# Performance work log

Hardware: AMD Instinct MI355X
Metric: run time of the kernel (lower is better)

The kernel has to match this reference:

```python
import jax, jax.numpy as jnp
import numpy as np

N_NODES, D_H, D_MSG, N_LAYERS = 512, 64, 64, 3
T, E = 128, 8192


def setup_inputs() -> dict:
    key = jax.random.key(0)
    ks = jax.random.split(key, 16)
    s = 0.1
    t = jax.random.uniform(ks[0], (T,), dtype=jnp.float32)
    edge_index = jax.random.randint(ks[1], (2, E), 0, N_NODES, dtype=jnp.int64)
    inp = {
        "t": t,
        "edge_index": edge_index,
        "enc_w": jax.random.normal(ks[2], (1 + N_NODES, D_H), jnp.float32) * s,
        "enc_b": jnp.zeros((D_H,), jnp.float32),
        "msg1_w": jax.random.normal(ks[3], (N_LAYERS, 2 * D_H, D_MSG), jnp.float32) * s,
        "msg1_b": jnp.zeros((N_LAYERS, D_MSG), jnp.float32),
        "msg2_w": jax.random.normal(ks[4], (N_LAYERS, D_MSG, D_MSG), jnp.float32) * s,
        "msg2_b": jnp.zeros((N_LAYERS, D_MSG), jnp.float32),
        "upd1_w": jax.random.normal(ks[5], (N_LAYERS, D_H + D_MSG, D_H), jnp.float32) * s,
        "upd1_b": jnp.zeros((N_LAYERS, D_H), jnp.float32),
        "upd2_w": jax.random.normal(ks[6], (N_LAYERS, D_H, D_H), jnp.float32) * s,
        "upd2_b": jnp.zeros((N_LAYERS, D_H), jnp.float32),
        "ro_w": jax.random.normal(ks[7], (D_H, 1), jnp.float32) * s,
        "ro_b": jnp.zeros((1,), jnp.float32),
    }
    return inp


def reference(t, edge_index, enc_w, enc_b, msg1_w, msg1_b, msg2_w, msg2_b,
              upd1_w, upd1_b, upd2_w, upd2_b, ro_w, ro_b):
    Tn = t.shape[0]
    N = enc_w.shape[0] - 1
    L = msg1_w.shape[0]
    # node features: [t, one_hot(node_id)] -> encode
    t_feat = jnp.broadcast_to(t[:, None, None], (Tn, N, 1))          # [T,N,1]
    id_feat = jnp.broadcast_to(jnp.eye(N, dtype=t.dtype), (Tn, N, N))  # [T,N,N]
    x = jnp.concatenate([t_feat, id_feat], axis=-1)                   # [T,N,1+N]
    h = x @ enc_w + enc_b                                             # [T,N,d_h]
    src, dst = edge_index[0], edge_index[1]
    for l in range(L):
        # message MLP on gathered [h_src, h_dst]
        cat = jnp.concatenate([h[:, src], h[:, dst]], axis=-1)        # [T,E,2*d_h]
        m = jax.nn.silu(cat @ msg1_w[l] + msg1_b[l]) @ msg2_w[l] + msg2_b[l]  # [T,E,d_msg]
        # scatter-add into destination nodes (index_add)
        agg = jnp.zeros((Tn, N, m.shape[-1]), dtype=h.dtype).at[:, dst].add(m)
        u = jnp.concatenate([h, agg], axis=-1)                        # [T,N,d_h+d_msg]
        upd = jax.nn.silu(u @ upd1_w[l] + upd1_b[l]) @ upd2_w[l] + upd2_b[l]
        h = h + upd                                                   # residual
    out = (h @ ro_w + ro_b)[..., 0]                                   # [T,N]
    return out
```

## Files before the change

kernel.cpp:

```cpp
#include <hip/hip_runtime.h>

#define TT 128
#define NN 512
#define DH 64
#define EE 8192
#define LOB (18 * 8 * 64)

typedef __bf16 bf16x8 __attribute__((ext_vector_type(8)));
typedef float f32x4 __attribute__((ext_vector_type(4)));

struct US8 { unsigned short u[8]; };
struct Frag { bf16x8 hi, lo; };

static __device__ __forceinline__ unsigned short f2bf(float x) {
    union { float f; unsigned u; } c; c.f = x;
    unsigned r = (c.u + 0x7FFFu + ((c.u >> 16) & 1u)) >> 16;
    return (unsigned short)r;
}
static __device__ __forceinline__ float bf2f(unsigned short b) {
    union { unsigned u; float f; } c; c.u = ((unsigned)b) << 16;
    return c.f;
}
static __device__ __forceinline__ float silu_acc(float a, float b, float acc) {
    float x = a + b;
    float e = __expf(-x);
    return fmaf(x, __builtin_amdgcn_rcpf(1.0f + e), acc);
}
static __device__ __forceinline__ float silu_f(float x) {
    float e = __expf(-x);
    return x * __builtin_amdgcn_rcpf(1.0f + e);
}
static __device__ __forceinline__ Frag split8(const float* v) {
    Frag f;
    #pragma unroll
    for (int i = 0; i < 8; ++i) {
        __bf16 hb = (__bf16)v[i];
        f.hi[i] = hb;
        f.lo[i] = (__bf16)(v[i] - (float)hb);
    }
    return f;
}
static __device__ __forceinline__ f32x4 mmac(bf16x8 a, uint4 bw, f32x4 c) {
    return __builtin_amdgcn_mfma_f32_16x16x32_bf16(
        a, __builtin_bit_cast(bf16x8, bw), c, 0, 0, 0);
}
static __device__ __forceinline__ f32x4 mm3(Frag a, uint4 wh, uint4 wl, f32x4 c) {
    c = mmac(a.hi, wh, c);
    c = mmac(a.lo, wh, c);
    c = mmac(a.hi, wl, c);
    return c;
}

__global__ __launch_bounds__(512) void setup_kernel(
    const int* __restrict__ ei,
    const float* __restrict__ msg1_w, const float* __restrict__ msg2_w,
    const float* __restrict__ upd1_w, const float* __restrict__ upd2_w,
    const float* __restrict__ msg2_b,
    const float* __restrict__ enc_w, const float* __restrict__ enc_b,
    const float* __restrict__ msg1_b,
    uint4* __restrict__ pack,
    int* __restrict__ counts, int* __restrict__ offsets,
    int* __restrict__ ssrc,
    float* __restrict__ E1s, float* __restrict__ E1d,
    float* __restrict__ e0sum, float* __restrict__ c2) {
    int b = blockIdx.x;
    if (b < 18) {
        int l = b / 6, bi = b % 6;
        const float* W;
        if (bi == 0)      W = msg1_w + (size_t)l * 128 * 64;
        else if (bi == 1) W = msg1_w + (size_t)l * 128 * 64 + 64 * 64;
        else if (bi == 3) W = upd1_w + (size_t)l * 128 * 64;
        else if (bi == 4) W = upd1_w + (size_t)l * 128 * 64 + 64 * 64;
        else if (bi == 5) W = upd2_w + (size_t)l * 64 * 64;
        else              W = nullptr;
        __shared__ float Gs[64 * 64];
        if (bi == 2) {
            const float* W2  = msg2_w + (size_t)l * 64 * 64;
            const float* U1b = upd1_w + (size_t)l * 128 * 64 + 64 * 64;
            int k = threadIdx.x >> 3;
            int dbase = (threadIdx.x & 7) * 8;
            float acc[8] = {0.f, 0.f, 0.f, 0.f, 0.f, 0.f, 0.f, 0.f};
            for (int j = 0; j < 64; ++j) {
                float a = W2[k * 64 + j];
                #pragma unroll
                for (int i = 0; i < 8; ++i)
                    acc[i] = fmaf(a, U1b[j * 64 + dbase + i], acc[i]);
            }
            #pragma unroll
            for (int i = 0; i < 8; ++i) Gs[k * 64 + dbase + i] = acc[i];
            if (threadIdx.x < 64) {
                int d = threadIdx.x;
                float s = 0.f;
                for (int j = 0; j < 64; ++j)
                    s = fmaf(msg2_b[l * 64 + j], U1b[j * 64 + d], s);
                c2[l * 64 + d] = s;
            }
            __syncthreads();
            W = Gs;
        }
        int lane = threadIdx.x & 63;
        int sub  = threadIdx.x >> 6;
        int nt = sub >> 1, kc = sub & 1;
        US8 oh, ol;
        #pragma unroll
        for (int i = 0; i < 8; ++i) {
            int k = kc * 32 + (lane >> 4) * 8 + i;
            int col = nt * 16 + (lane & 15);
            float w = W[k * 64 + col];
            unsigned short hu = f2bf(w);
            oh.u[i] = hu;
            ol.u[i] = f2bf(w - bf2f(hu));
        }
        size_t fi = ((size_t)b * 8 + sub) * 64 + lane;
        pack[fi]       = __builtin_bit_cast(uint4, oh);
        pack[LOB + fi] = __builtin_bit_cast(uint4, ol);
        return;
    }
    if (b == 18) {
        __shared__ int cnt[NN];
        __shared__ int tmp[NN];
        __shared__ int cur[NN];
        int i = threadIdx.x;
        cnt[i] = 0;
        __syncthreads();
        #pragma unroll
        for (int r = 0; r < EE / 512; ++r)
            atomicAdd(&cnt[ei[EE + r * 512 + i]], 1);
        __syncthreads();
        int c = cnt[i];
        tmp[i] = c;
        __syncthreads();
        for (int off = 1; off < NN; off <<= 1) {
            int v = (i >= off) ? tmp[i - off] : 0;
            __syncthreads();
            tmp[i] += v;
            __syncthreads();
        }
        counts[i] = c;
        offsets[i + 1] = tmp[i];
        if (i == 0) offsets[0] = 0;
        cur[i] = tmp[i] - c;
        __syncthreads();
        #pragma unroll
        for (int r = 0; r < EE / 512; ++r) {
            int e = r * 512 + i;
            int dst = ei[EE + e];
            int pos = atomicAdd(&cur[dst], 1);
            ssrc[pos] = ei[e];
        }
        return;
    }
    if (b < 83) {
        int nn = (b - 19) * 8 + (threadIdx.x >> 6);
        int d  = threadIdx.x & 63;
        float s = 0.f, dd = msg1_b[d];
        #pragma unroll 8
        for (int k = 0; k < 64; ++k) {
            float c = enc_w[(1 + nn) * 64 + k] + enc_b[k];
            s  = fmaf(c, msg1_w[k * 64 + d], s);
            dd = fmaf(c, msg1_w[(64 + k) * 64 + d], dd);
        }
        E1s[nn * 64 + d] = s;
        E1d[nn * 64 + d] = dd;
        return;
    }
    if (threadIdx.x < 64) {
        int d = threadIdx.x;
        float s = 0.f, dd = 0.f;
        #pragma unroll 8
        for (int k = 0; k < 64; ++k) {
            float a = enc_w[k];
            s  = fmaf(a, msg1_w[k * 64 + d], s);
            dd = fmaf(a, msg1_w[(64 + k) * 64 + d], dd);
        }
        e0sum[d] = s + dd;
    }
}

static __device__ __forceinline__ int swz_rowbase(int bid, int w) {
    int xcd = bid & 7;
    int idx = bid >> 3;
    int tt  = xcd * 16 + (idx >> 3);
    int sub = idx & 7;
    return tt * NN + sub * 64 + w * 16;
}

#define AGG_BODY(GB, BASE)                                                     \
    float4 acc = make_float4(0.f, 0.f, 0.f, 0.f);                              \
    int i = beg + eg;                                                          \
    for (; i + 4 < end; i += 8) {                                              \
        int s0 = ssrc[i] << 8;                                                 \
        int s1 = ssrc[i + 4] << 8;                                             \
        float4 v0 = *(const float4*)(GB + s0 + ch4);                           \
        float4 v1 = *(const float4*)(GB + s1 + ch4);                           \
        acc.x = silu_acc(v0.x, BASE.x, acc.x);                                 \
        acc.y = silu_acc(v0.y, BASE.y, acc.y);                                 \
        acc.z = silu_acc(v0.z, BASE.z, acc.z);                                 \
        acc.w = silu_acc(v0.w, BASE.w, acc.w);                                 \
        acc.x = silu_acc(v1.x, BASE.x, acc.x);                                 \
        acc.y = silu_acc(v1.y, BASE.y, acc.y);                                 \
        acc.z = silu_acc(v1.z, BASE.z, acc.z);                                 \
        acc.w = silu_acc(v1.w, BASE.w, acc.w);                                 \
    }                                                                          \
    if (i < end) {                                                             \
        int s0 = ssrc[i] << 8;                                                 \
        float4 v0 = *(const float4*)(GB + s0 + ch4);                           \
        acc.x = silu_acc(v0.x, BASE.x, acc.x);                                 \
        acc.y = silu_acc(v0.y, BASE.y, acc.y);                                 \
        acc.z = silu_acc(v0.z, BASE.z, acc.z);                                 \
        acc.w = silu_acc(v0.w, BASE.w, acc.w);                                 \
    }                                                                          \
    acc.x += __shfl_xor(acc.x, 16); acc.x += __shfl_xor(acc.x, 32);            \
    acc.y += __shfl_xor(acc.y, 16); acc.y += __shfl_xor(acc.y, 32);            \
    acc.z += __shfl_xor(acc.z, 16); acc.z += __shfl_xor(acc.z, 32);            \
    acc.w += __shfl_xor(acc.w, 16); acc.w += __shfl_xor(acc.w, 32);

__global__ __launch_bounds__(256) void agg0_kernel(
    const float* __restrict__ t, const float* __restrict__ e0sum,
    const float* __restrict__ E1s, const float* __restrict__ E1d,
    const int* __restrict__ offsets, const int* __restrict__ ssrc,
    float* __restrict__ aggpre) {
    int bid = blockIdx.x;
    int xcd = bid & 7;
    int idx = bid >> 3;
    int tt  = xcd * 16 + (idx >> 7);
    int n   = (idx & 127) * 4 + (threadIdx.x >> 6);
    int lane = threadIdx.x & 63;
    int eg = lane >> 4;
    int chb = (lane & 15) * 4;
    int ch4 = chb * 4;
    float tv = t[tt];
    float4 e0 = *(const float4*)(e0sum + chb);
    float4 ed = *(const float4*)(E1d + n * DH + chb);
    float4 base = make_float4(fmaf(tv, e0.x, ed.x), fmaf(tv, e0.y, ed.y),
                              fmaf(tv, e0.z, ed.z), fmaf(tv, e0.w, ed.w));
    int beg = offsets[n], end = offsets[n + 1];
    const char* Eb = (const char*)E1s;
    AGG_BODY(Eb, base)
    if (eg == 0)
        *(float4*)(aggpre + ((size_t)tt * NN + n) * DH + chb) = acc;
}

__global__ __launch_bounds__(256) void agg_kernel(
    const float* __restrict__ hs, const float* __restrict__ hd,
    const int* __restrict__ offsets, const int* __restrict__ ssrc,
    float* __restrict__ aggpre) {
    int bid = blockIdx.x;
    int xcd = bid & 7;
    int idx = bid >> 3;
    int tt  = xcd * 16 + (idx >> 7);
    int n   = (idx & 127) * 4 + (threadIdx.x >> 6);
    int lane = threadIdx.x & 63;
    size_t rowoff = ((size_t)tt * NN + n) * DH;
    int eg = lane >> 4;
    int chb = (lane & 15) * 4;
    int ch4 = chb * 4;
    float4 hdv = *(const float4*)(hd + rowoff + chb);
    int beg = offsets[n], end = offsets[n + 1];
    const char* hb = (const char*)(hs + (size_t)tt * NN * DH);
    AGG_BODY(hb, hdv)
    if (eg == 0) *(float4*)(aggpre + rowoff + chb) = acc;
}

__global__ __launch_bounds__(256) void upd_mfma_kernel(
    float* __restrict__ h, const float* __restrict__ aggpre,
    const float* __restrict__ t, const float* __restrict__ enc_w,
    const float* __restrict__ enc_b,
    const int* __restrict__ counts, const uint4* __restrict__ pack, int l,
    const float* __restrict__ c2, const float* __restrict__ ub1,
    const float* __restrict__ ub2, const float* __restrict__ b1n,
    float* __restrict__ hs, float* __restrict__ hd,
    const float* __restrict__ ro_w, const float* __restrict__ ro_b,
    float* __restrict__ out, int first, int last) {
    __shared__ float tile[4][16 * 68];
    int lane = threadIdx.x & 63;
    int w = threadIdx.x >> 6;
    int rowbase = swz_rowbase(blockIdx.x, w);
    float* TA = tile[w];
    int arow = lane & 15, kgrp = lane >> 4, k0 = kgrp * 8;
    int hrow = rowbase + arow;

    float hf[16];
    if (first) {
        int n = (rowbase & (NN - 1)) + arow;
        float tv = t[rowbase >> 9];
        #pragma unroll
        for (int kc = 0; kc < 2; ++kc)
            #pragma unroll
            for (int i = 0; i < 8; ++i) {
                int k = kc * 32 + k0 + i;
                hf[kc * 8 + i] = tv * enc_w[k] + enc_w[(1 + n) * DH + k] + enc_b[k];
            }
    } else {
        *(float4*)&hf[0]  = *(const float4*)(h + (size_t)hrow * DH + k0);
        *(float4*)&hf[4]  = *(const float4*)(h + (size_t)hrow * DH + k0 + 4);
        *(float4*)&hf[8]  = *(const float4*)(h + (size_t)hrow * DH + 32 + k0);
        *(float4*)&hf[12] = *(const float4*)(h + (size_t)hrow * DH + 32 + k0 + 4);
    }
    Frag ha0 = split8(&hf[0]), ha1 = split8(&hf[8]);

    float gf[16];
    *(float4*)&gf[0]  = *(const float4*)(aggpre + (size_t)hrow * DH + k0);
    *(float4*)&gf[4]  = *(const float4*)(aggpre + (size_t)hrow * DH + k0 + 4);
    *(float4*)&gf[8]  = *(const float4*)(aggpre + (size_t)hrow * DH + 32 + k0);
    *(float4*)&gf[12] = *(const float4*)(aggpre + (size_t)hrow * DH + 32 + k0 + 4);
    Frag ga0 = split8(&gf[0]), ga1 = split8(&gf[8]);

    const uint4* PGH  = pack + (size_t)(l * 6 + 2) * 512;
    const uint4* PGL  = PGH + LOB;
    const uint4* PU1tH = pack + (size_t)(l * 6 + 3) * 512;
    const uint4* PU1tL = PU1tH + LOB;
    const float* c2l = c2 + l * 64;
    float degv[4];
    #pragma unroll
    for (int r = 0; r < 4; ++r)
        degv[r] = (float)counts[(rowbase + kgrp * 4 + r) & (NN - 1)];
    #pragma unroll
    for (int nt = 0; nt < 4; ++nt) {
        float bv  = ub1[nt * 16 + (lane & 15)];
        float c2v = c2l[nt * 16 + (lane & 15)];
        f32x4 a;
        #pragma unroll
        for (int r = 0; r < 4; ++r) a[r] = fmaf(degv[r], c2v, bv);
        a = mm3(ha0, PU1tH[(nt * 2 + 0) * 64 + lane], PU1tL[(nt * 2 + 0) * 64 + lane], a);
        a = mm3(ha1, PU1tH[(nt * 2 + 1) * 64 + lane], PU1tL[(nt * 2 + 1) * 64 + lane], a);
        a = mm3(ga0, PGH[(nt * 2 + 0) * 64 + lane], PGL[(nt * 2 + 0) * 64 + lane], a);
        a = mm3(ga1, PGH[(nt * 2 + 1) * 64 + lane], PGL[(nt * 2 + 1) * 64 + lane], a);
        #pragma unroll
        for (int r = 0; r < 4; ++r)
            TA[(kgrp * 4 + r) * 68 + nt * 16 + (lane & 15)] = silu_f(a[r]);
    }
    float zb[16];
    #pragma unroll
    for (int i = 0; i < 8; ++i) zb[i] = TA[arow * 68 + k0 + i];
    #pragma unroll
    for (int i = 0; i < 8; ++i) zb[8 + i] = TA[arow * 68 + 32 + k0 + i];
    Frag kz0 = split8(&zb[0]), kz1 = split8(&zb[8]);

    const uint4* PU2H = pack + (size_t)(l * 6 + 5) * 512;
    const uint4* PU2L = PU2H + LOB;
    #pragma unroll
    for (int nt = 0; nt < 4; ++nt) {
        float bv = ub2[nt * 16 + (lane & 15)];
        f32x4 a;
        #pragma unroll
        for (int r = 0; r < 4; ++r) a[r] = bv;
        a = mm3(kz0, PU2H[(nt * 2 + 0) * 64 + lane], PU2L[(nt * 2 + 0) * 64 + lane], a);
        a = mm3(kz1, PU2H[(nt * 2 + 1) * 64 + lane], PU2L[(nt * 2 + 1) * 64 + lane], a);
        #pragma unroll
        for (int r = 0; r < 4; ++r)
            TA[(kgrp * 4 + r) * 68 + nt * 16 + (lane & 15)] = a[r];
    }
    float hn[16];
    #pragma unroll
    for (int i = 0; i < 8; ++i) hn[i] = hf[i] + TA[arow * 68 + k0 + i];
    #pragma unroll
    for (int i = 0; i < 8; ++i) hn[8 + i] = hf[8 + i] + TA[arow * 68 + 32 + k0 + i];

    if (last) {
        float v = 0.f;
        #pragma unroll
        for (int i = 0; i < 8; ++i) v += hn[i] * ro_w[k0 + i];
        #pragma unroll
        for (int i = 0; i < 8; ++i) v += hn[8 + i] * ro_w[32 + k0 + i];
        v += __shfl_xor(v, 16);
        v += __shfl_xor(v, 32);
        if (lane < 16) out[rowbase + lane] = v + ro_b[0];
        return;
    }

    *(float4*)(h + (size_t)hrow * DH + k0) = make_float4(hn[0], hn[1], hn[2], hn[3]);
    *(float4*)(h + (size_t)hrow * DH + k0 + 4) = make_float4(hn[4], hn[5], hn[6], hn[7]);
    *(float4*)(h + (size_t)hrow * DH + 32 + k0) = make_float4(hn[8], hn[9], hn[10], hn[11]);
    *(float4*)(h + (size_t)hrow * DH + 32 + k0 + 4) = make_float4(hn[12], hn[13], hn[14], hn[15]);

    Frag na0 = split8(&hn[0]), na1 = split8(&hn[8]);
    const uint4* PWtH = pack + (size_t)((l + 1) * 6 + 0) * 512;
    const uint4* PWbH = pack + (size_t)((l + 1) * 6 + 1) * 512;
    const uint4* PWtL = PWtH + LOB;
    const uint4* PWbL = PWbH + LOB;
    #pragma unroll
    for (int nt = 0; nt < 4; ++nt) {
        f32x4 s; f32x4 d;
        float b1v = b1n[nt * 16 + (lane & 15)];
        #pragma unroll
        for (int r = 0; r < 4; ++r) { s[r] = 0.f; d[r] = b1v; }
        s = mm3(na0, PWtH[(nt * 2 + 0) * 64 + lane], PWtL[(nt * 2 + 0) * 64 + lane], s);
        s = mm3(na1, PWtH[(nt * 2 + 1) * 64 + lane], PWtL[(nt * 2 + 1) * 64 + lane], s);
        d = mm3(na0, PWbH[(nt * 2 + 0) * 64 + lane], PWbL[(nt * 2 + 0) * 64 + lane], d);
        d = mm3(na1, PWbH[(nt * 2 + 1) * 64 + lane], PWbL[(nt * 2 + 1) * 64 + lane], d);
        #pragma unroll
        for (int r = 0; r < 4; ++r) {
            int rr = rowbase + kgrp * 4 + r;
            hs[(size_t)rr * DH + nt * 16 + (lane & 15)] = s[r];
            hd[(size_t)rr * DH + nt * 16 + (lane & 15)] = d[r];
        }
    }
}

extern "C" void kernel_launch(void* const* d_in, const int* in_sizes, int n_in,
                              void* d_out, int out_size, void* d_ws, size_t ws_size,
                              hipStream_t stream) {
    const float* t      = (const float*)d_in[0];
    const int*   ei     = (const int*)d_in[1];
    const float* enc_w  = (const float*)d_in[2];
    const float* enc_b  = (const float*)d_in[3];
    const float* msg1_w = (const float*)d_in[4];
    const float* msg1_b = (const float*)d_in[5];
    const float* msg2_w = (const float*)d_in[6];
    const float* msg2_b = (const float*)d_in[7];
    const float* upd1_w = (const float*)d_in[8];
    const float* upd1_b = (const float*)d_in[9];
    const float* upd2_w = (const float*)d_in[10];
    const float* upd2_b = (const float*)d_in[11];
    const float* ro_w   = (const float*)d_in[12];
    const float* ro_b   = (const float*)d_in[13];
    float* out = (float*)d_out;

    const size_t HN = (size_t)TT * NN * DH;
    float* h      = (float*)d_ws;
    float* hs     = h + HN;
    float* hd     = hs + HN;
    float* aggpre = hd + HN;
    uint4* pack   = (uint4*)(aggpre + HN);
    int* counts  = (int*)(pack + 2 * LOB);
    int* offsets = counts + NN;
    int* ssrc    = offsets + NN + 1;
    float* E1s   = (float*)(ssrc + EE);
    float* E1d   = E1s + NN * DH;
    float* e0sum = E1d + NN * DH;
    float* c2    = e0sum + DH;

    setup_kernel<<<84, 512, 0, stream>>>(ei, msg1_w, msg2_w, upd1_w, upd2_w,
                                         msg2_b, enc_w, enc_b, msg1_b,
                                         pack, counts, offsets, ssrc,
                                         E1s, E1d, e0sum, c2);

    for (int l = 0; l < 3; ++l) {
        if (l == 0)
            agg0_kernel<<<TT * NN / 4, 256, 0, stream>>>(
                t, e0sum, E1s, E1d, offsets, ssrc, aggpre);
        else
            agg_kernel<<<TT * NN / 4, 256, 0, stream>>>(
                hs, hd, offsets, ssrc, aggpre);
        int last = (l == 2);
        upd_mfma_kernel<<<TT * NN / 64, 256, 0, stream>>>(
            h, aggpre, t, enc_w, enc_b, counts, pack, l,
            c2, upd1_b + (size_t)l * DH,
            upd2_b + (size_t)l * DH,
            last ? msg1_b : msg1_b + (size_t)(l + 1) * DH,
            hs, hd, ro_w, ro_b, out, (l == 0) ? 1 : 0, last);
    }
}
```

Measured before the change: 266.6 us.

## Fuse all GNN layers into one persistent cooperative kernel with grid sync

```diff
diff --git a/kernel.cpp b/kernel.cpp
--- a/kernel.cpp
+++ b/kernel.cpp
@@ -1,4 +1,7 @@
 #include <hip/hip_runtime.h>
+#include <hip/hip_cooperative_groups.h>
+
+namespace cg = cooperative_groups;
 
 #define TT 128
 #define NN 512
@@ -215,6 +218,175 @@
     acc.z += __shfl_xor(acc.z, 16); acc.z += __shfl_xor(acc.z, 32);            \
     acc.w += __shfl_xor(acc.w, 16); acc.w += __shfl_xor(acc.w, 32);
 
+__global__ __launch_bounds__(512, 4) void gnn_coop(
+    const float* __restrict__ t, const float* __restrict__ enc_w,
+    const float* __restrict__ enc_b, const uint4* __restrict__ pack,
+    const int* __restrict__ counts, const int* __restrict__ offsets,
+    const int* __restrict__ ssrc,
+    const float* __restrict__ E1s, const float* __restrict__ E1d,
+    const float* __restrict__ e0sum,
+    float* __restrict__ hsA, float* __restrict__ hsB,
+    float* __restrict__ hd,
+    const float* __restrict__ msg1_b, const float* __restrict__ upd1_b,
+    const float* __restrict__ upd2_b, const float* __restrict__ c2,
+    const float* __restrict__ ro_w, const float* __restrict__ ro_b,
+    float* __restrict__ out) {
+    cg::grid_group grid = cg::this_grid();
+    __shared__ float tile[8][16 * 68];
+    int lane = threadIdx.x & 63;
+    int w = threadIdx.x >> 6;
+    int bid = blockIdx.x;
+    int xcd = bid & 7;
+    int idx = bid >> 3;
+    int tt  = xcd * 16 + (idx >> 2);
+    int quarter = idx & 3;
+    int rowbase = tt * NN + quarter * 128 + w * 16;
+    int nbase = rowbase & (NN - 1);
+    float* TA = tile[w];
+    int arow = lane & 15, kgrp = lane >> 4, k0 = kgrp * 8;
+    float tv = t[tt];
+
+    float hv[16];
+    {
+        int n = nbase + arow;
+        #pragma unroll
+        for (int kc = 0; kc < 2; ++kc)
+            #pragma unroll
+            for (int i = 0; i < 8; ++i) {
+                int k = kc * 32 + k0 + i;
+                hv[kc * 8 + i] = tv * enc_w[k] + enc_w[(1 + n) * DH + k] + enc_b[k];
+            }
+    }
+
+    const float* hs_in = hsA;
+    float* hs_out = hsA;
+
+    for (int l = 0; l < 3; ++l) {
+        int first = (l == 0), last = (l == 2);
+
+        {
+            int eg = lane >> 4;
+            int chb = (lane & 15) * 4;
+            int ch4 = chb * 4;
+            const char* gb = first ? (const char*)E1s
+                                   : (const char*)(hs_in + (size_t)tt * NN * DH);
+            for (int j = 0; j < 16; ++j) {
+                int nn = nbase + j;
+                float4 base;
+                if (first) {
+                    float4 e0 = *(const float4*)(e0sum + chb);
+                    float4 ed = *(const float4*)(E1d + nn * DH + chb);
+                    base = make_float4(fmaf(tv, e0.x, ed.x), fmaf(tv, e0.y, ed.y),
+                                       fmaf(tv, e0.z, ed.z), fmaf(tv, e0.w, ed.w));
+                } else {
+                    base = *(const float4*)(hd + ((size_t)tt * NN + nn) * DH + chb);
+                }
+                int beg = offsets[nn], end = offsets[nn + 1];
+                AGG_BODY(gb, base)
+                if (eg == 0) *(float4*)(&TA[j * 68 + chb]) = acc;
+            }
+        }
+
+        float gf[16];
+        #pragma unroll
+        for (int i = 0; i < 8; ++i) gf[i] = TA[arow * 68 + k0 + i];
+        #pragma unroll
+        for (int i = 0; i < 8; ++i) gf[8 + i] = TA[arow * 68 + 32 + k0 + i];
+        Frag ga0 = split8(&gf[0]), ga1 = split8(&gf[8]);
+        Frag ha0 = split8(&hv[0]), ha1 = split8(&hv[8]);
+
+        const uint4* PGH   = pack + (size_t)(l * 6 + 2) * 512;
+        const uint4* PGL   = PGH + LOB;
+        const uint4* PU1tH = pack + (size_t)(l * 6 + 3) * 512;
+        const uint4* PU1tL = PU1tH + LOB;
+        const float* c2l = c2 + l * 64;
+        const float* ub1 = upd1_b + l * 64;
+        float degv[4];
+        #pragma unroll
+        for (int r = 0; r < 4; ++r)
+            degv[r] = (float)counts[nbase + kgrp * 4 + r];
+        #pragma unroll
+        for (int nt = 0; nt < 4; ++nt) {
+            float bv  = ub1[nt * 16 + (lane & 15)];
+            float c2v = c2l[nt * 16 + (lane & 15)];
+            f32x4 a;
+            #pragma unroll
+            for (int r = 0; r < 4; ++r) a[r] = fmaf(degv[r], c2v, bv);
+            a = mm3(ha0, PU1tH[(nt * 2 + 0) * 64 + lane], PU1tL[(nt * 2 + 0) * 64 + lane], a);
+            a = mm3(ha1, PU1tH[(nt * 2 + 1) * 64 + lane], PU1tL[(nt * 2 + 1) * 64 + lane], a);
+            a = mm3(ga0, PGH[(nt * 2 + 0) * 64 + lane], PGL[(nt * 2 + 0) * 64 + lane], a);
+            a = mm3(ga1, PGH[(nt * 2 + 1) * 64 + lane], PGL[(nt * 2 + 1) * 64 + lane], a);
+            #pragma unroll
+            for (int r = 0; r < 4; ++r)
+                TA[(kgrp * 4 + r) * 68 + nt * 16 + (lane & 15)] = silu_f(a[r]);
+        }
+        float zb[16];
+        #pragma unroll
+        for (int i = 0; i < 8; ++i) zb[i] = TA[arow * 68 + k0 + i];
+        #pragma unroll
+        for (int i = 0; i < 8; ++i) zb[8 + i] = TA[arow * 68 + 32 + k0 + i];
+        Frag kz0 = split8(&zb[0]), kz1 = split8(&zb[8]);
+
+        const uint4* PU2H = pack + (size_t)(l * 6 + 5) * 512;
+        const uint4* PU2L = PU2H + LOB;
+        const float* ub2 = upd2_b + l * 64;
+        #pragma unroll
+        for (int nt = 0; nt < 4; ++nt) {
+            float bv = ub2[nt * 16 + (lane & 15)];
+            f32x4 a;
+            #pragma unroll
+            for (int r = 0; r < 4; ++r) a[r] = bv;
+            a = mm3(kz0, PU2H[(nt * 2 + 0) * 64 + lane], PU2L[(nt * 2 + 0) * 64 + lane], a);
+            a = mm3(kz1, PU2H[(nt * 2 + 1) * 64 + lane], PU2L[(nt * 2 + 1) * 64 + lane], a);
+            #pragma unroll
+            for (int r = 0; r < 4; ++r)
+                TA[(kgrp * 4 + r) * 68 + nt * 16 + (lane & 15)] = a[r];
+        }
+        #pragma unroll
+        for (int i = 0; i < 8; ++i) hv[i] += TA[arow * 68 + k0 + i];
+        #pragma unroll
+        for (int i = 0; i < 8; ++i) hv[8 + i] += TA[arow * 68 + 32 + k0 + i];
+
+        if (last) {
+            float v = 0.f;
+            #pragma unroll
+            for (int i = 0; i < 8; ++i) v += hv[i] * ro_w[k0 + i];
+            #pragma unroll
+            for (int i = 0; i < 8; ++i) v += hv[8 + i] * ro_w[32 + k0 + i];
+            v += __shfl_xor(v, 16);
+            v += __shfl_xor(v, 32);
+            if (lane < 16) out[rowbase + lane] = v + ro_b[0];
+        } else {
+            Frag na0 = split8(&hv[0]), na1 = split8(&hv[8]);
+            const uint4* PWtH = pack + (size_t)((l + 1) * 6 + 0) * 512;
+            const uint4* PWbH = pack + (size_t)((l + 1) * 6 + 1) * 512;
+            const uint4* PWtL = PWtH + LOB;
+            const uint4* PWbL = PWbH + LOB;
+            const float* b1n = msg1_b + (size_t)(l + 1) * DH;
+            #pragma unroll
+            for (int nt = 0; nt < 4; ++nt) {
+                f32x4 s; f32x4 d;
+                float b1v = b1n[nt * 16 + (lane & 15)];
+                #pragma unroll
+                for (int r = 0; r < 4; ++r) { s[r] = 0.f; d[r] = b1v; }
+                s = mm3(na0, PWtH[(nt * 2 + 0) * 64 + lane], PWtL[(nt * 2 + 0) * 64 + lane], s);
+                s = mm3(na1, PWtH[(nt * 2 + 1) * 64 + lane], PWtL[(nt * 2 + 1) * 64 + lane], s);
+                d = mm3(na0, PWbH[(nt * 2 + 0) * 64 + lane], PWbL[(nt * 2 + 0) * 64 + lane], d);
+                d = mm3(na1, PWbH[(nt * 2 + 1) * 64 + lane], PWbL[(nt * 2 + 1) * 64 + lane], d);
+                #pragma unroll
+                for (int r = 0; r < 4; ++r) {
+                    int rr = rowbase + kgrp * 4 + r;
+                    hs_out[(size_t)rr * DH + nt * 16 + (lane & 15)] = s[r];
+                    hd[(size_t)rr * DH + nt * 16 + (lane & 15)] = d[r];
+                }
+            }
+            grid.sync();
+            hs_in = hs_out;
+            hs_out = (hs_out == hsA) ? hsB : hsA;
+        }
+    }
+}
+
 __global__ __launch_bounds__(256) void agg0_kernel(
     const float* __restrict__ t, const float* __restrict__ e0sum,
     const float* __restrict__ E1s, const float* __restrict__ E1d,
@@ -436,6 +608,29 @@
                                          pack, counts, offsets, ssrc,
                                          E1s, E1d, e0sum, c2);
 
+    const uint4* packc = pack;
+    const int* countsc = counts;
+    const int* offsetsc = offsets;
+    const int* ssrcc = ssrc;
+    const float* E1sc = E1s;
+    const float* E1dc = E1d;
+    const float* e0sumc = e0sum;
+    const float* c2c = c2;
+    float* hsA = hs;
+    float* hsB = aggpre;
+    void* args[] = {
+        (void*)&t, (void*)&enc_w, (void*)&enc_b, (void*)&packc,
+        (void*)&countsc, (void*)&offsetsc, (void*)&ssrcc,
+        (void*)&E1sc, (void*)&E1dc, (void*)&e0sumc,
+        (void*)&hsA, (void*)&hsB, (void*)&hd,
+        (void*)&msg1_b, (void*)&upd1_b, (void*)&upd2_b, (void*)&c2c,
+        (void*)&ro_w, (void*)&ro_b, (void*)&out
+    };
+    hipError_t cerr = hipLaunchCooperativeKernel(
+        (const void*)gnn_coop, dim3(512), dim3(512), args, 0, stream);
+    if (cerr == hipSuccess) return;
+    (void)hipGetLastError();
+
     for (int l = 0; l < 3; ++l) {
         if (l == 0)
             agg0_kernel<<<TT * NN / 4, 256, 0, stream>>>(
```

Measured after the change: 427.6 us. +60.4%, slower.
